# Kernel tuning notes

Measured on AMD Instinct MI355X. Metric: run time of the kernel, lower is better.

Reference implementation:

```python
import jax, jax.numpy as jnp
import numpy as np

H, L, NH, DH, FF, V, MAXP = 768, 2, 12, 64, 3072, 50265, 512
B, S = 64, 512


def _ln(x, g, b, eps=1e-5):
    mu = jnp.mean(x, axis=-1, keepdims=True)
    var = jnp.mean(jnp.square(x - mu), axis=-1, keepdims=True)
    return (x - mu) * jax.lax.rsqrt(var + eps) * g + b


def setup_inputs() -> dict:
    key = jax.random.key(0)
    ks = jax.random.split(key, 16)
    sd = 0.02
    inp = {
        "source_ids": jax.random.randint(ks[0], (B, S), 0, V),
        "position_idx": jax.random.randint(ks[1], (B, S), 0, MAXP),
        "attn_mask": jax.random.randint(ks[2], (B, S, S), 0, 2).astype(bool),
        "word_emb": sd * jax.random.normal(ks[3], (V, H), jnp.float32),
        "pos_emb": sd * jax.random.normal(ks[4], (MAXP, H), jnp.float32),
        "ln_g": jnp.ones((H,), jnp.float32),
        "ln_b": jnp.zeros((H,), jnp.float32),
        "Wqkv": sd * jax.random.normal(ks[5], (L, H, 3 * H), jnp.float32),
        "bqkv": jnp.zeros((L, 3 * H), jnp.float32),
        "Wo": sd * jax.random.normal(ks[6], (L, H, H), jnp.float32),
        "bo": jnp.zeros((L, H), jnp.float32),
        "ln1_g": jnp.ones((L, H), jnp.float32),
        "ln1_b": jnp.zeros((L, H), jnp.float32),
        "W1": sd * jax.random.normal(ks[7], (L, H, FF), jnp.float32),
        "b1": jnp.zeros((L, FF), jnp.float32),
        "W2": sd * jax.random.normal(ks[8], (L, FF, H), jnp.float32),
        "b2": jnp.zeros((L, H), jnp.float32),
        "ln2_g": jnp.ones((L, H), jnp.float32),
        "ln2_b": jnp.zeros((L, H), jnp.float32),
        "dense_W": sd * jax.random.normal(ks[9], (H, H), jnp.float32),
        "dense_b": jnp.zeros((H,), jnp.float32),
        "out_W": sd * jax.random.normal(ks[10], (H, 1), jnp.float32),
        "out_b": jnp.zeros((1,), jnp.float32),
    }
    return inp


def reference(source_ids, position_idx, attn_mask, word_emb, pos_emb, ln_g, ln_b,
              Wqkv, bqkv, Wo, bo, ln1_g, ln1_b, W1, b1, W2, b2, ln2_g, ln2_b,
              dense_W, dense_b, out_W, out_b):
    nodes_mask = position_idx == 0          # [B,S] bool
    token_mask = position_idx >= 2          # [B,S] bool
    emb = word_emb[source_ids]              # [B,S,H]

    # node -> token masked mean aggregation (the custom-kernel hotspot)
    m = (nodes_mask[:, :, None] & token_mask[:, None, :] & attn_mask).astype(emb.dtype)  # [B,S,S]
    w = m / (jnp.sum(m, axis=-1, keepdims=True) + 1e-10)
    avg = jnp.einsum('bnt,btd->bnd', w, emb)
    nm = nodes_mask[:, :, None].astype(emb.dtype)
    emb = emb * (1.0 - nm) + avg * nm

    # RoBERTa-style embeddings: inputs_embeds + position embeddings, layernorm
    h = _ln(emb + pos_emb[position_idx], ln_g, ln_b)

    # additive attention bias from 3D mask
    bias = jnp.where(attn_mask, 0.0, -1e4).astype(h.dtype)[:, None, :, :]  # [B,1,S,S]
    scale = 1.0 / np.sqrt(DH)

    for l in range(L):
        qkv = h @ Wqkv[l] + bqkv[l]                     # [B,S,3H]
        q, k, v = jnp.split(qkv, 3, axis=-1)
        q = q.reshape(B, S, NH, DH)
        k = k.reshape(B, S, NH, DH)
        v = v.reshape(B, S, NH, DH)
        scores = jnp.einsum('bqhd,bkhd->bhqk', q, k) * scale + bias
        attn = jax.nn.softmax(scores, axis=-1)
        ctx = jnp.einsum('bhqk,bkhd->bqhd', attn, v).reshape(B, S, H)
        h = _ln(h + ctx @ Wo[l] + bo[l], ln1_g[l], ln1_b[l])
        ffn = jax.nn.gelu(h @ W1[l] + b1[l], approximate=False) @ W2[l] + b2[l]
        h = _ln(h + ffn, ln2_g[l], ln2_b[l])

    # classification head (dropout in eval = identity)
    x = h[:, 0, :]
    x = jnp.tanh(x @ dense_W + dense_b)
    logits = x @ out_W + out_b                          # [B,1]
    return logits
```

## Files before the change

kernel.cpp:

```cpp
#include <hip/hip_runtime.h>

typedef unsigned short u16;
typedef unsigned int   u32;
typedef __bf16 bf16x8 __attribute__((ext_vector_type(8)));
typedef float  f32x4  __attribute__((ext_vector_type(4)));

#define DEVI __device__ __forceinline__

DEVI u16 f2bf(float f){
  u32 u = __builtin_bit_cast(u32, f);
  u32 r = (u + 0x7fffu + ((u >> 16) & 1u)) >> 16;
  return (u16)r;
}
DEVI float bf2f(u16 u){
  u32 x = ((u32)u) << 16;
  return __builtin_bit_cast(float, x);
}

DEVI void gload16(const void* g, void* lds){
  __builtin_amdgcn_global_load_lds(
      (const __attribute__((address_space(1))) void*)g,
      (__attribute__((address_space(3))) void*)lds, 16, 0, 0);
}

DEVI f32x4 MFMA(bf16x8 a, bf16x8 b, f32x4 c){
  return __builtin_amdgcn_mfma_f32_16x16x32_bf16(a, b, c, 0, 0, 0);
}

#define BAR() do { asm volatile("s_barrier" ::: "memory"); \
                   __builtin_amdgcn_sched_barrier(0); } while(0)

__global__ void k_maskprobe(const unsigned char* __restrict__ m, int* __restrict__ flag){
  __shared__ int s;
  if (threadIdx.x == 0) s = 0;
  __syncthreads();
  int acc = 0;
  for (int i = threadIdx.x; i < 65536; i += 256)
    if ((i & 3) != 0 && m[i] != 0) acc++;
  atomicAdd(&s, acc);
  __syncthreads();
  if (threadIdx.x == 0) *flag = (s > 0) ? 1 : 0;
}

__global__ void k_maskbits(const void* __restrict__ mask, const int* __restrict__ flag,
                           u32* __restrict__ mb){
  int row  = blockIdx.x * 4 + (threadIdx.x >> 6);
  int lane = threadIdx.x & 63;
  bool bytes = (*flag != 0);
  for (int c0 = 0; c0 < 512; c0 += 64){
    int v;
    if (bytes) v = ((const unsigned char*)mask)[(size_t)row * 512 + c0 + lane];
    else       v = ((const int*)mask)[(size_t)row * 512 + c0 + lane];
    unsigned long long bits = __ballot(v != 0);
    if (lane == 0){
      mb[(size_t)row * 16 + (c0 >> 5)]     = (u32)(bits & 0xffffffffull);
      mb[(size_t)row * 16 + (c0 >> 5) + 1] = (u32)(bits >> 32);
    }
  }
}

__global__ void k_embln(const int* __restrict__ ids, const int* __restrict__ pos,
                        const u32* __restrict__ mb, const float* __restrict__ wemb,
                        const float* __restrict__ pemb, const float* __restrict__ g,
                        const float* __restrict__ be, u16* __restrict__ hb){
  __shared__ float s1[4], s2[4];
  int row = blockIdx.x, t = threadIdx.x;
  int p = pos[row];
  float x0, x1, x2;
  if (p == 0){
    int b = row >> 9;
    const u32* mrow = mb + (size_t)row * 16;
    const int* pb = pos + ((size_t)b << 9);
    const int* ib = ids + ((size_t)b << 9);
    float a0 = 0.f, a1 = 0.f, a2 = 0.f, cnt = 0.f;
    #pragma unroll 8
    for (int k = 0; k < 512; k++){
      float w = (pb[k] >= 2 && ((mrow[k >> 5] >> (k & 31)) & 1)) ? 1.f : 0.f;
      const float* src = wemb + (size_t)ib[k] * 768;
      a0 += w * src[t]; a1 += w * src[t+256]; a2 += w * src[t+512];
      cnt += w;
    }
    float inv = 1.f / (cnt + 1e-10f);
    x0 = a0 * inv; x1 = a1 * inv; x2 = a2 * inv;
  } else {
    const float* src = wemb + (size_t)ids[row] * 768;
    x0 = src[t]; x1 = src[t+256]; x2 = src[t+512];
  }
  const float* pr = pemb + (size_t)p * 768;
  x0 += pr[t]; x1 += pr[t+256]; x2 += pr[t+512];
  float s = x0 + x1 + x2, q = x0*x0 + x1*x1 + x2*x2;
  for (int o = 32; o; o >>= 1){ s += __shfl_down(s, o, 64); q += __shfl_down(q, o, 64); }
  int wv = t >> 6, ln = t & 63;
  if (!ln){ s1[wv] = s; s2[wv] = q; }
  __syncthreads();
  s = s1[0]+s1[1]+s1[2]+s1[3]; q = s2[0]+s2[1]+s2[2]+s2[3];
  float mu = s * (1.f/768.f);
  float rs = rsqrtf(q * (1.f/768.f) - mu*mu + 1e-5f);
  u16* hbr = hb + (size_t)row * 768;
  hbr[t]     = f2bf((x0-mu)*rs*g[t]     + be[t]);
  hbr[t+256] = f2bf((x1-mu)*rs*g[t+256] + be[t+256]);
  hbr[t+512] = f2bf((x2-mu)*rs*g[t+512] + be[t+512]);
}

__global__ void k_lnres(const u16* __restrict__ C, const float* __restrict__ g,
                        const float* __restrict__ be, u16* __restrict__ hb){
  __shared__ float s1[4], s2[4];
  int row = blockIdx.x, t = threadIdx.x;
  u16* hr = hb + (size_t)row * 768;
  const u16* cr = C + (size_t)row * 768;
  float x0 = bf2f(hr[t])     + bf2f(cr[t]);
  float x1 = bf2f(hr[t+256]) + bf2f(cr[t+256]);
  float x2 = bf2f(hr[t+512]) + bf2f(cr[t+512]);
  float s = x0 + x1 + x2, q = x0*x0 + x1*x1 + x2*x2;
  for (int o = 32; o; o >>= 1){ s += __shfl_down(s, o, 64); q += __shfl_down(q, o, 64); }
  int wv = t >> 6, ln = t & 63;
  if (!ln){ s1[wv] = s; s2[wv] = q; }
  __syncthreads();
  s = s1[0]+s1[1]+s1[2]+s1[3]; q = s2[0]+s2[1]+s2[2]+s2[3];
  float mu = s * (1.f/768.f);
  float rs = rsqrtf(q * (1.f/768.f) - mu*mu + 1e-5f);
  hr[t]     = f2bf((x0-mu)*rs*g[t]     + be[t]);
  hr[t+256] = f2bf((x1-mu)*rs*g[t+256] + be[t+256]);
  hr[t+512] = f2bf((x2-mu)*rs*g[t+512] + be[t+512]);
}

__global__ void k_transpose(const float* __restrict__ src, u16* __restrict__ dst,
                            int K, int N){
  __shared__ float tile[32][33];
  int k0 = blockIdx.x * 32, n0 = blockIdx.y * 32;
  int tx = threadIdx.x & 31, ty = threadIdx.x >> 5;
  #pragma unroll
  for (int i = 0; i < 32; i += 8)
    tile[ty + i][tx] = src[(size_t)(k0 + ty + i) * N + n0 + tx];
  __syncthreads();
  #pragma unroll
  for (int i = 0; i < 32; i += 8)
    dst[(size_t)(n0 + ty + i) * K + k0 + tx] = f2bf(tile[tx][ty + i]);
}

DEVI void stageA32(const u16* __restrict__ src, int K, u16* lds, int tid){
  int r = tid >> 2, c = tid & 3;
  int sc = c ^ ((r >> 1) & 3);
  gload16(src + (size_t)r*K + sc*8, lds + (size_t)tid*8);
}
DEVI void stageB32(const u16* __restrict__ src, int K, u16* lds, int tid){
  #pragma unroll
  for (int j = 0; j < 2; j++){
    int p = j*512 + tid;
    int r = p >> 2, c = p & 3;
    int sc = c ^ ((r >> 1) & 3);
    gload16(src + (size_t)r*K + sc*8, lds + (size_t)p*8);
  }
}

template<int EPI>
__global__ __launch_bounds__(512, 4)
void k_gemm3(const u16* __restrict__ A, const u16* __restrict__ BT,
             const float* __restrict__ bias, void* __restrict__ out,
             void* __restrict__ out2, int M, int N, int K){
  __shared__ __align__(16) u16 sm[36864];
  const int tid = threadIdx.x;
  const int w = tid >> 6, lane = tid & 63;
  const int wm = w >> 2, wn = w & 3;
  const int cr = lane & 15, cg = lane >> 4;

  const int nbn = gridDim.x;
  const int nwg = nbn * gridDim.y;
  const int d   = blockIdx.y * nbn + blockIdx.x;
  const int xcd = d & 7, qq = nwg >> 3, rr = nwg & 7;
  const int logical = (xcd < rr ? xcd*(qq+1) : rr*(qq+1) + (xcd-rr)*qq) + (d >> 3);
  const int m0 = (logical / nbn) * 128;
  const int n0 = (logical % nbn) * 256;

  const int NT = K >> 5;
  const u16* Abase = A  + (size_t)m0 * K;
  const u16* Bbase = BT + (size_t)n0 * K;
  const int rowA = wm*64 + cr;
  const int rowB = wn*64 + cr;

  f32x4 acc[4][4] = {};
  bf16x8 afr[4], bfr[4];

  stageA32(Abase, K, sm, tid);
  stageB32(Bbase, K, sm + 12288, tid);
  if (NT > 1){
    stageA32(Abase + 32, K, sm + 4096, tid);
    stageB32(Bbase + 32, K, sm + 12288 + 8192, tid);
    asm volatile("s_waitcnt vmcnt(3)" ::: "memory");
  } else {
    asm volatile("s_waitcnt vmcnt(0)" ::: "memory");
  }
  __builtin_amdgcn_sched_barrier(0);
  BAR();

  int bcur = 0;
  for (int t = 0; t < NT; ++t){
    const int ab = bcur << 12;
    const int bb = 12288 + (bcur << 13);
    int bn2 = bcur + 2; if (bn2 >= 3) bn2 -= 3;

    #pragma unroll
    for (int n = 0; n < 4; n++){
      int r = rowB + n*16;
      bfr[n] = *(const bf16x8*)&sm[bb + r*32 + ((cg ^ ((r >> 1) & 3)) << 3)];
    }
    #pragma unroll
    for (int i = 0; i < 4; i++){
      int r = rowA + i*16;
      afr[i] = *(const bf16x8*)&sm[ab + r*32 + ((cg ^ ((r >> 1) & 3)) << 3)];
    }
    if (t + 2 < NT){
      stageA32(Abase + (size_t)(t+2)*32, K, sm + (bn2 << 12), tid);
      stageB32(Bbase + (size_t)(t+2)*32, K, sm + 12288 + (bn2 << 13), tid);
    }

    __builtin_amdgcn_s_setprio(1);
    #pragma unroll
    for (int i = 0; i < 4; i++)
      #pragma unroll
      for (int n = 0; n < 4; n++)
        acc[i][n] = MFMA(afr[i], bfr[n], acc[i][n]);
    __builtin_amdgcn_s_setprio(0);

    if (t + 2 < NT) { asm volatile("s_waitcnt vmcnt(3)" ::: "memory"); }
    else            { asm volatile("s_waitcnt vmcnt(0)" ::: "memory"); }
    __builtin_amdgcn_sched_barrier(0);
    BAR();
    bcur = bcur + 1; if (bcur >= 3) bcur = 0;
  }

  if (EPI == 1){
    #pragma unroll
    for (int n = 0; n < 4; n++){
      int col = n0 + wn*64 + n*16 + cr;
      float bv = bias[col];
      #pragma unroll
      for (int i = 0; i < 4; i++){
        #pragma unroll
        for (int j = 0; j < 4; j++){
          int row = m0 + wm*64 + i*16 + cg*4 + j;
          ((float*)out)[(size_t)row * N + col] = acc[i][n][j] + bv;
        }
      }
    }
  } else {
    const bool vblk = (EPI == 3) && (n0 >= 1536);
    const int LDC = vblk ? 266 : 264;
    #pragma unroll
    for (int n = 0; n < 4; n++){
      int coll = wn*64 + n*16 + cr;
      float bv = bias[n0 + coll];
      #pragma unroll
      for (int i = 0; i < 4; i++){
        #pragma unroll
        for (int j = 0; j < 4; j++){
          int rowl = wm*64 + i*16 + cg*4 + j;
          float v = acc[i][n][j] + bv;
          if (EPI == 2) v = 0.5f * v * (1.f + erff(v * 0.70710678118654752f));
          sm[rowl*LDC + coll] = f2bf(v);
        }
      }
    }
    BAR();
    if (EPI == 3){
      int b = m0 >> 9, s0 = m0 & 511;
      if (vblk){
        int hd0 = (n0 - 1536) >> 6;
        int dl = lane >> 2, sc4 = lane & 3;
        #pragma unroll
        for (int it = 0; it < 8; it++){
          int gidx = it*8 + w;
          int hh2 = gidx >> 4, dhi = (gidx >> 2) & 3, shi = gidx & 3;
          int dd2 = dhi*16 + dl;
          int schunk = shi*4 + sc4;
          u16 tmp[8];
          #pragma unroll
          for (int k = 0; k < 8; k++)
            tmp[k] = sm[(schunk*8 + k)*266 + hh2*64 + dd2];
          *(uint4*)((u16*)out2 + (((size_t)(b*12 + hd0 + hh2)*64 + dd2) << 9)
                    + s0 + schunk*8) = *(uint4*)tmp;
        }
      } else {
        #pragma unroll
        for (int it = 0; it < 8; it++){
          int idx = it*512 + tid;
          int c = idx & 7, hh2 = (idx >> 3) & 3, s = idx >> 5;
          uint4 v4 = *(const uint4*)&sm[s*264 + hh2*64 + c*8];
          int col0 = n0 + hh2*64;
          int sec = (col0 >= 768) ? 1 : 0;
          int hd  = (col0 - sec*768) >> 6;
          *(uint4*)((u16*)out + (size_t)sec*25165824 +
                    (((size_t)(b*12 + hd)*512 + (m0 & 511) + s) << 6) + c*8) = v4;
        }
      }
    } else {
      #pragma unroll
      for (int it = 0; it < 8; it++){
        int idx = it*512 + tid;
        int r = idx >> 5, c8 = idx & 31;
        uint4 v4 = *(const uint4*)&sm[r*264 + c8*8];
        *(uint4*)((u16*)out + (size_t)(m0 + r)*N + n0 + c8*8) = v4;
      }
    }
  }
}

DEVI void stage64(const u16* __restrict__ src, int stride, u16* lds, int w, int lane){
  #pragma unroll
  for (int j = 0; j < 2; j++){
    int p  = j*256 + w*64 + lane;
    int r  = p >> 3;
    int c8 = (p & 7) ^ (r & 7);
    gload16(src + (size_t)r*stride + c8*8, lds + (size_t)p*8);
  }
}

__global__ __launch_bounds__(256, 4)
void k_attn3(const u16* __restrict__ qp, const u16* __restrict__ kp,
             const u16* __restrict__ vt, const u32* __restrict__ mb,
             u16* __restrict__ ctx){
  __shared__ __align__(16) u16 Ks[8192];
  __shared__ __align__(16) u16 Vs[8192];
  const int tid = threadIdx.x, wv = tid >> 6, lane = tid & 63;
  const int cr = lane & 15, cg = lane >> 4;
  const int cg4 = cg * 4;
  const int r7 = cr & 7;

  const int dd = blockIdx.x + (blockIdx.y << 3);
  const int logical = (dd & 7) * 768 + (dd >> 3);
  const int bh = logical >> 3;
  const int qblk = logical & 7;
  const int b = bh / 12, hh = bh % 12;
  const int qw = qblk * 64 + wv * 16;
  const int qrow = qw + cr;
  const size_t base = (size_t)bh * 512 * 64;
  const u16* vtb = vt + (size_t)bh * 64 * 512;

  const int slot0 = ((cg    ) ^ r7) << 3;
  const int slot1 = ((4 + cg) ^ r7) << 3;

  bf16x8 qB[2];
  #pragma unroll
  for (int ks = 0; ks < 2; ks++)
    qB[ks] = *(const bf16x8*)&qp[base + (size_t)qrow * 64 + ks*32 + cg*8];

  u32 mw[16];
  {
    const u32* mrow = mb + ((size_t)b * 512 + qrow) * 16;
    #pragma unroll
    for (int i = 0; i < 4; i++){
      uint4 v4 = *(const uint4*)&mrow[i*4];
      mw[i*4+0] = v4.x; mw[i*4+1] = v4.y; mw[i*4+2] = v4.z; mw[i*4+3] = v4.w;
    }
  }

  stage64(kp + base, 64, Ks, wv, lane);
  stage64(vtb,      512, Vs, wv, lane);
  asm volatile("s_waitcnt vmcnt(0)" ::: "memory");
  __builtin_amdgcn_sched_barrier(0);
  BAR();

  float m = -3e38f, vs = 0.f;
  f32x4 oacc[4] = {};

  for (int s = 0; s < 8; ++s){
    const int buf = (s & 1) << 12;
    const int nbf = ((s + 1) & 1) << 12;

    if (s + 1 < 8){
      stage64(kp + base + (size_t)(s+1)*4096, 64, Ks + nbf, wv, lane);
      stage64(vtb + (size_t)(s+1)*64,        512, Vs + nbf, wv, lane);
    }

    f32x4 pacc[4];
    #pragma unroll
    for (int tt = 0; tt < 4; tt++){
      bf16x8 a0 = *(const bf16x8*)&Ks[buf + (tt*16 + cr)*64 + slot0];
      bf16x8 a1 = *(const bf16x8*)&Ks[buf + (tt*16 + cr)*64 + slot1];
      f32x4 z = {0.f, 0.f, 0.f, 0.f};
      z = MFMA(a0, qB[0], z);
      z = MFMA(a1, qB[1], z);
      pacc[tt] = z;
    }

    const u32 w0 = mw[2*s], w1 = mw[2*s+1];
    f32x4 vmx = {-3e38f, -3e38f, -3e38f, -3e38f};
    #pragma unroll
    for (int tt = 0; tt < 4; tt++){
      u32 nib = (((tt < 2) ? w0 : w1) >> (16*(tt & 1) + cg4)) & 0xFu;
      #pragma unroll
      for (int j = 0; j < 4; j++){
        float v = pacc[tt][j] * 0.125f + (((nib >> j) & 1u) ? 0.f : -10000.f);
        pacc[tt][j] = v;
        vmx[j] = fmaxf(vmx[j], v);
      }
    }
    float tm = fmaxf(fmaxf(vmx[0], vmx[1]), fmaxf(vmx[2], vmx[3]));
    tm = fmaxf(tm, __shfl_xor(tm, 16, 64));
    tm = fmaxf(tm, __shfl_xor(tm, 32, 64));

    float mnew = fmaxf(m, tm);
    float alpha = __expf(m - mnew);
    m = mnew;
    #pragma unroll
    for (int db = 0; db < 4; db++) oacc[db] *= alpha;

    f32x4 vsum = {0.f, 0.f, 0.f, 0.f};
    #pragma unroll
    for (int tt = 0; tt < 4; tt++){
      #pragma unroll
      for (int j = 0; j < 4; j++){
        float e = __expf(pacc[tt][j] - m);
        pacc[tt][j] = e;
        vsum[j] += e;
      }
    }
    vs = vs * alpha + (vsum[0] + vsum[1] + vsum[2] + vsum[3]);

    bf16x8 pa[2];
    #pragma unroll
    for (int c = 0; c < 2; c++)
      #pragma unroll
      for (int e = 0; e < 4; e++){
        pa[c][e]   = (__bf16)pacc[2*c][e];
        pa[c][4+e] = (__bf16)pacc[2*c+1][e];
      }

    #pragma unroll
    for (int c = 0; c < 2; c++){
      const int ch0 = ((4*c     + (cg >> 1)) ^ r7);
      const int ch1 = ((4*c + 2 + (cg >> 1)) ^ r7);
      const int sub = (cg & 1) << 3;
      #pragma unroll
      for (int db = 0; db < 4; db++){
        const char* vrow = (const char*)&Vs[buf + (db*16 + cr)*64];
        bf16x8 vb;
        ((uint2*)&vb)[0] = *(const uint2*)(vrow + (ch0 << 4) + sub);
        ((uint2*)&vb)[1] = *(const uint2*)(vrow + (ch1 << 4) + sub);
        oacc[db] = MFMA(pa[c], vb, oacc[db]);
      }
    }

    if (s + 1 < 8) { asm volatile("s_waitcnt vmcnt(0)" ::: "memory"); }
    __builtin_amdgcn_sched_barrier(0);
    BAR();
  }

  vs += __shfl_xor(vs, 16, 64);
  vs += __shfl_xor(vs, 32, 64);
  #pragma unroll
  for (int j = 0; j < 4; j++){
    float ds = __shfl(vs, cg4 + j, 64);
    float inv = 1.0f / ds;
    #pragma unroll
    for (int db = 0; db < 4; db++)
      ctx[((size_t)b * 512 + qw + cg4 + j) * 768 + hh*64 + 16*db + cr] = f2bf(oacc[db][j] * inv);
  }
}

__global__ __launch_bounds__(256)
void k_dense(const u16* __restrict__ hb, const float* __restrict__ W,
             const float* __restrict__ bias, float* __restrict__ xt){
  __shared__ float xs[768];
  __shared__ float red[256];
  const int b = blockIdx.y, t = threadIdx.x;
  const u16* hr = hb + (size_t)b * 512 * 768;
  xs[t] = bf2f(hr[t]); xs[t+256] = bf2f(hr[t+256]); xs[t+512] = bf2f(hr[t+512]);
  __syncthreads();
  const int col = blockIdx.x * 64 + (t & 63);
  const int ks  = t >> 6;
  const float* Wp = W + (size_t)(ks * 192) * 768 + col;
  const float* xp = xs + ks * 192;
  float a = 0.f;
  #pragma unroll 8
  for (int k = 0; k < 192; k++) a += xp[k] * Wp[(size_t)k * 768];
  red[t] = a;
  __syncthreads();
  if (t < 64){
    float y = red[t] + red[t+64] + red[t+128] + red[t+192] + bias[col];
    xt[(size_t)b * 768 + col] = tanhf(y);
  }
}

__global__ void k_logits(const float* __restrict__ xt, const float* __restrict__ ow,
                         const float* __restrict__ ob, float* __restrict__ out){
  __shared__ float sb[4];
  int b = blockIdx.x, t = threadIdx.x;
  const float* x = xt + (size_t)b * 768;
  float s = x[t]*ow[t] + x[t+256]*ow[t+256] + x[t+512]*ow[t+512];
  for (int o = 32; o; o >>= 1) s += __shfl_down(s, o, 64);
  int wv = t >> 6, ln = t & 63;
  if (!ln) sb[wv] = s;
  __syncthreads();
  if (t == 0) out[b] = sb[0] + sb[1] + sb[2] + sb[3] + ob[0];
}

extern "C" void kernel_launch(void* const* d_in, const int* in_sizes, int n_in,
                              void* d_out, int out_size, void* d_ws, size_t ws_size,
                              hipStream_t stream){
  if (n_in < 23) return;
  if (ws_size < 534000000ull) return;

  const int*   ids  = (const int*)  d_in[0];
  const int*   pos  = (const int*)  d_in[1];
  const void*  amsk =               d_in[2];
  const float* wemb = (const float*)d_in[3];
  const float* pemb = (const float*)d_in[4];
  const float* lng  = (const float*)d_in[5];
  const float* lnb  = (const float*)d_in[6];
  const float* Wqkv = (const float*)d_in[7];
  const float* bqkv = (const float*)d_in[8];
  const float* Wo   = (const float*)d_in[9];
  const float* bo   = (const float*)d_in[10];
  const float* ln1g = (const float*)d_in[11];
  const float* ln1b = (const float*)d_in[12];
  const float* W1   = (const float*)d_in[13];
  const float* b1   = (const float*)d_in[14];
  const float* W2   = (const float*)d_in[15];
  const float* b2   = (const float*)d_in[16];
  const float* ln2g = (const float*)d_in[17];
  const float* ln2b = (const float*)d_in[18];
  const float* dW   = (const float*)d_in[19];
  const float* db   = (const float*)d_in[20];
  const float* oW   = (const float*)d_in[21];
  const float* ob   = (const float*)d_in[22];

  char* ws = (char*)d_ws;
  u16*   hb   = (u16*)  (ws + 100663296);
  u16*   C    = (u16*)  (ws + 150994944);
  u16*   qkvp = (u16*)  (ws + 251658240);
  u16*   vt   = (u16*)  (ws + 402653184);
  u16*   act  = (u16*)  (ws + 251658240);
  u16*   ctx  = (u16*)  (ws + 452984832);
  u32*   mbit = (u32*)  (ws + 503316480);
  u16*   wt   = (u16*)  (ws + 505413632);
  float* xt   = (float*)(ws + 533725184);
  int*   flag = (int*)  (ws + 533921792);

  u16* qp   = qkvp;
  u16* kp   = qkvp + (size_t)25165824;

  u16* WqkvT = wt;
  u16* WoT   = WqkvT + (size_t)2*2304*768;
  u16* W1T   = WoT   + (size_t)2*768*768;
  u16* W2T   = W1T   + (size_t)2*3072*768;

  k_maskprobe<<<1, 256, 0, stream>>>((const unsigned char*)amsk, flag);
  k_maskbits<<<8192, 256, 0, stream>>>(amsk, flag, mbit);

  for (int l = 0; l < 2; l++){
    k_transpose<<<dim3(24, 72), 256, 0, stream>>>(Wqkv + (size_t)l*768*2304, WqkvT + (size_t)l*2304*768, 768, 2304);
    k_transpose<<<dim3(24, 24), 256, 0, stream>>>(Wo   + (size_t)l*768*768,  WoT   + (size_t)l*768*768,  768, 768);
    k_transpose<<<dim3(24, 96), 256, 0, stream>>>(W1   + (size_t)l*768*3072, W1T   + (size_t)l*3072*768, 768, 3072);
    k_transpose<<<dim3(96, 24), 256, 0, stream>>>(W2   + (size_t)l*3072*768, W2T   + (size_t)l*768*3072, 3072, 768);
  }

  k_embln<<<32768, 256, 0, stream>>>(ids, pos, mbit, wemb, pemb, lng, lnb, hb);

  for (int l = 0; l < 2; l++){
    k_gemm3<3><<<dim3(9, 256), 512, 0, stream>>>(hb, WqkvT + (size_t)l*2304*768, bqkv + l*2304, (void*)qkvp, (void*)vt, 32768, 2304, 768);
    k_attn3<<<dim3(8, 768), 256, 0, stream>>>(qp, kp, vt, mbit, ctx);
    k_gemm3<0><<<dim3(3, 256), 512, 0, stream>>>(ctx, WoT + (size_t)l*768*768, bo + l*768, (void*)C, nullptr, 32768, 768, 768);
    k_lnres<<<32768, 256, 0, stream>>>(C, ln1g + l*768, ln1b + l*768, hb);
    k_gemm3<2><<<dim3(12, 256), 512, 0, stream>>>(hb, W1T + (size_t)l*3072*768, b1 + l*3072, (void*)act, nullptr, 32768, 3072, 768);
    k_gemm3<0><<<dim3(3, 256), 512, 0, stream>>>(act, W2T + (size_t)l*768*3072, b2 + l*768, (void*)C, nullptr, 32768, 768, 3072);
    k_lnres<<<32768, 256, 0, stream>>>(C, ln2g + l*768, ln2b + l*768, hb);
  }

  k_dense<<<dim3(12, 64), 256, 0, stream>>>(hb, dW, db, xt);
  k_logits<<<64, 256, 0, stream>>>(xt, oW, ob, (float*)d_out);
}
```

Measured before the change: 1.708 ms.

## Enlarge GEMM tiles to 256x256 with K=64 double-buffered interleaved staging

Replaces the 128x256, K=32 triple-buffered GEMM with a 256x256 tile over K=64 steps. Each wave now holds 8x4 MFMA accumulators, and A/B half-tiles are staged in four phases interleaved with MFMA groups into 128KB of LDS. The aim is more reuse per loaded byte and fewer K iterations. The costs are higher register and LDS pressure (launch bounds drop to 2 waves per SIMD), extra barriers, a two-pass epilogue, and half as many workgroups, which may hurt occupancy on small N grids.

```diff
diff --git a/kernel.cpp b/kernel.cpp
--- a/kernel.cpp
+++ b/kernel.cpp
@@ -138,27 +138,26 @@
     dst[(size_t)(n0 + ty + i) * K + k0 + tx] = f2bf(tile[tx][ty + i]);
 }
 
-DEVI void stageA32(const u16* __restrict__ src, int K, u16* lds, int tid){
-  int r = tid >> 2, c = tid & 3;
-  int sc = c ^ ((r >> 1) & 3);
-  gload16(src + (size_t)r*K + sc*8, lds + (size_t)tid*8);
-}
-DEVI void stageB32(const u16* __restrict__ src, int K, u16* lds, int tid){
+
+DEVI void stage_half(const u16* __restrict__ P, int row0, int K, int kt, int h,
+                     int boff, u16* sm, int w, int lane){
   #pragma unroll
   for (int j = 0; j < 2; j++){
-    int p = j*512 + tid;
-    int r = p >> 2, c = p & 3;
-    int sc = c ^ ((r >> 1) & 3);
-    gload16(src + (size_t)r*K + sc*8, lds + (size_t)p*8);
+    int ob = ((w*2 + j) << 10);
+    int o  = ob + lane*16;
+    int r  = (h << 7) + (o >> 7);
+    int c  = ((o >> 4) & 7) ^ (r & 7);
+    gload16(P + (size_t)(row0 + r)*K + (size_t)kt*64 + c*8,
+            &sm[boff + (h << 13) + (ob >> 1)]);
   }
 }
 
 template<int EPI>
-__global__ __launch_bounds__(512, 4)
-void k_gemm3(const u16* __restrict__ A, const u16* __restrict__ BT,
+__global__ __launch_bounds__(512, 2)
+void k_gemm2(const u16* __restrict__ A, const u16* __restrict__ BT,
              const float* __restrict__ bias, void* __restrict__ out,
              void* __restrict__ out2, int M, int N, int K){
-  __shared__ __align__(16) u16 sm[36864];
+  __shared__ __align__(16) u16 sm[65536];
   const int tid = threadIdx.x;
   const int w = tid >> 6, lane = tid & 63;
   const int wm = w >> 2, wn = w & 3;
@@ -169,65 +168,87 @@
   const int d   = blockIdx.y * nbn + blockIdx.x;
   const int xcd = d & 7, qq = nwg >> 3, rr = nwg & 7;
   const int logical = (xcd < rr ? xcd*(qq+1) : rr*(qq+1) + (xcd-rr)*qq) + (d >> 3);
-  const int m0 = (logical / nbn) * 128;
+  const int m0 = (logical / nbn) * 256;
   const int n0 = (logical % nbn) * 256;
 
-  const int NT = K >> 5;
-  const u16* Abase = A  + (size_t)m0 * K;
-  const u16* Bbase = BT + (size_t)n0 * K;
-  const int rowA = wm*64 + cr;
-  const int rowB = wn*64 + cr;
-
-  f32x4 acc[4][4] = {};
-  bf16x8 afr[4], bfr[4];
-
-  stageA32(Abase, K, sm, tid);
-  stageB32(Bbase, K, sm + 12288, tid);
+  const int NT = K >> 6;
+  const int rowA = wm*128 + cr;
+  const int rowB = wn*64  + cr;
+  int slot[2];
+  slot[0] = ((cg     ^ (cr & 7)) << 3);
+  slot[1] = (((4+cg) ^ (cr & 7)) << 3);
+
+  f32x4 acc[8][4] = {};
+  bf16x8 bfr[4][2], afr[2][2];
+
+#define LOADA(mf0) \
+  _Pragma("unroll") for (int i = 0; i < 2; i++) \
+    _Pragma("unroll") for (int s = 0; s < 2; s++) \
+      afr[i][s] = *(const bf16x8*)&sm[ab + (rowA + ((mf0)+i)*16)*64 + slot[s]];
+
+#define FMA2(mf0) \
+  __builtin_amdgcn_s_setprio(1); \
+  _Pragma("unroll") for (int n = 0; n < 4; n++){ \
+    acc[(mf0)][n]   = MFMA(afr[0][0], bfr[n][0], acc[(mf0)][n]); \
+    acc[(mf0)][n]   = MFMA(afr[0][1], bfr[n][1], acc[(mf0)][n]); \
+    acc[(mf0)+1][n] = MFMA(afr[1][0], bfr[n][0], acc[(mf0)+1][n]); \
+    acc[(mf0)+1][n] = MFMA(afr[1][1], bfr[n][1], acc[(mf0)+1][n]); \
+  } \
+  __builtin_amdgcn_s_setprio(0);
+
+  stage_half(A,  m0, K, 0, 0, 0,     sm, w, lane);
+  stage_half(A,  m0, K, 0, 1, 0,     sm, w, lane);
+  stage_half(BT, n0, K, 0, 0, 32768, sm, w, lane);
+  stage_half(BT, n0, K, 0, 1, 32768, sm, w, lane);
   if (NT > 1){
-    stageA32(Abase + 32, K, sm + 4096, tid);
-    stageB32(Bbase + 32, K, sm + 12288 + 8192, tid);
-    asm volatile("s_waitcnt vmcnt(3)" ::: "memory");
+    stage_half(BT, n0, K, 1, 0, 32768+16384, sm, w, lane);
+    stage_half(BT, n0, K, 1, 1, 32768+16384, sm, w, lane);
+    asm volatile("s_waitcnt vmcnt(4)" ::: "memory");
   } else {
     asm volatile("s_waitcnt vmcnt(0)" ::: "memory");
   }
   __builtin_amdgcn_sched_barrier(0);
   BAR();
 
-  int bcur = 0;
   for (int t = 0; t < NT; ++t){
-    const int ab = bcur << 12;
-    const int bb = 12288 + (bcur << 13);
-    int bn2 = bcur + 2; if (bn2 >= 3) bn2 -= 3;
-
-    #pragma unroll
-    for (int n = 0; n < 4; n++){
-      int r = rowB + n*16;
-      bfr[n] = *(const bf16x8*)&sm[bb + r*32 + ((cg ^ ((r >> 1) & 3)) << 3)];
-    }
-    #pragma unroll
-    for (int i = 0; i < 4; i++){
-      int r = rowA + i*16;
-      afr[i] = *(const bf16x8*)&sm[ab + r*32 + ((cg ^ ((r >> 1) & 3)) << 3)];
-    }
-    if (t + 2 < NT){
-      stageA32(Abase + (size_t)(t+2)*32, K, sm + (bn2 << 12), tid);
-      stageB32(Bbase + (size_t)(t+2)*32, K, sm + 12288 + (bn2 << 13), tid);
-    }
-
-    __builtin_amdgcn_s_setprio(1);
-    #pragma unroll
-    for (int i = 0; i < 4; i++)
+    const int ab  = (t & 1) << 14;
+    const int bb  = 32768 + ab;
+    const int nb1 = ((t + 1) & 1) << 14;
+
+    #pragma unroll
+    for (int n = 0; n < 4; n++)
       #pragma unroll
-      for (int n = 0; n < 4; n++)
-        acc[i][n] = MFMA(afr[i], bfr[n], acc[i][n]);
-    __builtin_amdgcn_s_setprio(0);
-
-    if (t + 2 < NT) { asm volatile("s_waitcnt vmcnt(3)" ::: "memory"); }
+      for (int s = 0; s < 2; s++)
+        bfr[n][s] = *(const bf16x8*)&sm[bb + (rowB + n*16)*64 + slot[s]];
+    LOADA(0);
+    if (t + 1 < NT) stage_half(A, m0, K, t+1, 0, nb1, sm, w, lane);
+    BAR();
+    FMA2(0);
+    BAR();
+
+    LOADA(2);
+    if (t + 1 < NT) stage_half(A, m0, K, t+1, 1, nb1, sm, w, lane);
+    BAR();
+    FMA2(2);
+    BAR();
+
+    LOADA(4);
+    if (t + 2 < NT) stage_half(BT, n0, K, t+2, 0, bb, sm, w, lane);
+    BAR();
+    FMA2(4);
+    BAR();
+
+    LOADA(6);
+    if (t + 2 < NT) stage_half(BT, n0, K, t+2, 1, bb, sm, w, lane);
+    BAR();
+    FMA2(6);
+    if (t + 2 < NT) { asm volatile("s_waitcnt vmcnt(4)" ::: "memory"); }
     else            { asm volatile("s_waitcnt vmcnt(0)" ::: "memory"); }
     __builtin_amdgcn_sched_barrier(0);
     BAR();
-    bcur = bcur + 1; if (bcur >= 3) bcur = 0;
-  }
+  }
+#undef LOADA
+#undef FMA2
 
   if (EPI == 1){
     #pragma unroll
@@ -235,11 +256,11 @@
       int col = n0 + wn*64 + n*16 + cr;
       float bv = bias[col];
       #pragma unroll
-      for (int i = 0; i < 4; i++){
+      for (int mf = 0; mf < 8; mf++){
         #pragma unroll
         for (int j = 0; j < 4; j++){
-          int row = m0 + wm*64 + i*16 + cg*4 + j;
-          ((float*)out)[(size_t)row * N + col] = acc[i][n][j] + bv;
+          int row = m0 + wm*128 + mf*16 + cg*4 + j;
+          ((float*)out)[(size_t)row * N + col] = acc[mf][n][j] + bv;
         }
       }
     }
@@ -247,59 +268,66 @@
     const bool vblk = (EPI == 3) && (n0 >= 1536);
     const int LDC = vblk ? 266 : 264;
     #pragma unroll
-    for (int n = 0; n < 4; n++){
-      int coll = wn*64 + n*16 + cr;
-      float bv = bias[n0 + coll];
-      #pragma unroll
-      for (int i = 0; i < 4; i++){
+    for (int pass = 0; pass < 2; ++pass){
+      BAR();
+      if (wm == pass){
         #pragma unroll
-        for (int j = 0; j < 4; j++){
-          int rowl = wm*64 + i*16 + cg*4 + j;
-          float v = acc[i][n][j] + bv;
-          if (EPI == 2) v = 0.5f * v * (1.f + erff(v * 0.70710678118654752f));
-          sm[rowl*LDC + coll] = f2bf(v);
+        for (int n = 0; n < 4; n++){
+          int coll = wn*64 + n*16 + cr;
+          float bv = bias[n0 + coll];
+          #pragma unroll
+          for (int mf = 0; mf < 8; mf++){
+            #pragma unroll
+            for (int j = 0; j < 4; j++){
+              int rowl = mf*16 + cg*4 + j;
+              float v = acc[mf][n][j] + bv;
+              if (EPI == 2) v = 0.5f * v * (1.f + erff(v * 0.70710678118654752f));
+              sm[rowl*LDC + coll] = f2bf(v);
+            }
+          }
         }
       }
-    }
-    BAR();
-    if (EPI == 3){
-      int b = m0 >> 9, s0 = m0 & 511;
-      if (vblk){
-        int hd0 = (n0 - 1536) >> 6;
-        int dl = lane >> 2, sc4 = lane & 3;
-        #pragma unroll
-        for (int it = 0; it < 8; it++){
-          int gidx = it*8 + w;
-          int hh2 = gidx >> 4, dhi = (gidx >> 2) & 3, shi = gidx & 3;
-          int dd2 = dhi*16 + dl;
-          int schunk = shi*4 + sc4;
-          u16 tmp[8];
+      BAR();
+      const int mrow0 = m0 + pass*128;
+      if (EPI == 3){
+        int b = mrow0 >> 9, s0 = mrow0 & 511;
+        if (vblk){
+          int hd0 = (n0 - 1536) >> 6;
+          int dl = lane >> 2, sc4 = lane & 3;
           #pragma unroll
-          for (int k = 0; k < 8; k++)
-            tmp[k] = sm[(schunk*8 + k)*266 + hh2*64 + dd2];
-          *(uint4*)((u16*)out2 + (((size_t)(b*12 + hd0 + hh2)*64 + dd2) << 9)
-                    + s0 + schunk*8) = *(uint4*)tmp;
+          for (int it = 0; it < 8; it++){
+            int gidx = it*8 + w;
+            int hh2 = gidx >> 4, dhi = (gidx >> 2) & 3, shi = gidx & 3;
+            int dd2 = dhi*16 + dl;
+            int schunk = shi*4 + sc4;
+            u16 tmp[8];
+            #pragma unroll
+            for (int k = 0; k < 8; k++)
+              tmp[k] = sm[(schunk*8 + k)*266 + hh2*64 + dd2];
+            *(uint4*)((u16*)out2 + (((size_t)(b*12 + hd0 + hh2)*64 + dd2) << 9)
+                      + s0 + schunk*8) = *(uint4*)tmp;
+          }
+        } else {
+          #pragma unroll
+          for (int it = 0; it < 8; it++){
+            int idx = it*512 + tid;
+            int c = idx & 7, hh2 = (idx >> 3) & 3, s = idx >> 5;
+            uint4 v4 = *(const uint4*)&sm[s*264 + hh2*64 + c*8];
+            int col0 = n0 + hh2*64;
+            int sec = (col0 >= 768) ? 1 : 0;
+            int hd  = (col0 - sec*768) >> 6;
+            *(uint4*)((u16*)out + (size_t)sec*25165824 +
+                      (((size_t)(b*12 + hd)*512 + s0 + s) << 6) + c*8) = v4;
+          }
         }
       } else {
         #pragma unroll
         for (int it = 0; it < 8; it++){
           int idx = it*512 + tid;
-          int c = idx & 7, hh2 = (idx >> 3) & 3, s = idx >> 5;
-          uint4 v4 = *(const uint4*)&sm[s*264 + hh2*64 + c*8];
-          int col0 = n0 + hh2*64;
-          int sec = (col0 >= 768) ? 1 : 0;
-          int hd  = (col0 - sec*768) >> 6;
-          *(uint4*)((u16*)out + (size_t)sec*25165824 +
-                    (((size_t)(b*12 + hd)*512 + (m0 & 511) + s) << 6) + c*8) = v4;
+          int r = idx >> 5, c8 = idx & 31;
+          uint4 v4 = *(const uint4*)&sm[r*264 + c8*8];
+          *(uint4*)((u16*)out + (size_t)(mrow0 + r)*N + n0 + c8*8) = v4;
         }
-      }
-    } else {
-      #pragma unroll
-      for (int it = 0; it < 8; it++){
-        int idx = it*512 + tid;
-        int r = idx >> 5, c8 = idx & 31;
-        uint4 v4 = *(const uint4*)&sm[r*264 + c8*8];
-        *(uint4*)((u16*)out + (size_t)(m0 + r)*N + n0 + c8*8) = v4;
       }
     }
   }
@@ -558,12 +586,12 @@
   k_embln<<<32768, 256, 0, stream>>>(ids, pos, mbit, wemb, pemb, lng, lnb, hb);
 
   for (int l = 0; l < 2; l++){
-    k_gemm3<3><<<dim3(9, 256), 512, 0, stream>>>(hb, WqkvT + (size_t)l*2304*768, bqkv + l*2304, (void*)qkvp, (void*)vt, 32768, 2304, 768);
+    k_gemm2<3><<<dim3(9, 128), 512, 0, stream>>>(hb, WqkvT + (size_t)l*2304*768, bqkv + l*2304, (void*)qkvp, (void*)vt, 32768, 2304, 768);
     k_attn3<<<dim3(8, 768), 256, 0, stream>>>(qp, kp, vt, mbit, ctx);
-    k_gemm3<0><<<dim3(3, 256), 512, 0, stream>>>(ctx, WoT + (size_t)l*768*768, bo + l*768, (void*)C, nullptr, 32768, 768, 768);
+    k_gemm2<0><<<dim3(3, 128), 512, 0, stream>>>(ctx, WoT + (size_t)l*768*768, bo + l*768, (void*)C, nullptr, 32768, 768, 768);
     k_lnres<<<32768, 256, 0, stream>>>(C, ln1g + l*768, ln1b + l*768, hb);
-    k_gemm3<2><<<dim3(12, 256), 512, 0, stream>>>(hb, W1T + (size_t)l*3072*768, b1 + l*3072, (void*)act, nullptr, 32768, 3072, 768);
-    k_gemm3<0><<<dim3(3, 256), 512, 0, stream>>>(act, W2T + (size_t)l*768*3072, b2 + l*768, (void*)C, nullptr, 32768, 768, 3072);
+    k_gemm2<2><<<dim3(12, 128), 512, 0, stream>>>(hb, W1T + (size_t)l*3072*768, b1 + l*3072, (void*)act, nullptr, 32768, 3072, 768);
+    k_gemm2<0><<<dim3(3, 128), 512, 0, stream>>>(act, W2T + (size_t)l*768*3072, b2 + l*768, (void*)C, nullptr, 32768, 768, 3072);
     k_lnres<<<32768, 256, 0, stream>>>(C, ln2g + l*768, ln2b + l*768, hb);
   }
 
```

Result: slower. 1.998 ms (+16.9%).
